# Optimization experiments

Measured on AMD Instinct MI355X. Metric: run time of the kernel, lower is better.

The kernel has to match this reference:

```python
import jax, jax.numpy as jnp
import numpy as np

C_ELEC = 322.0637  # Coulomb constant in Rosetta units


def _atom_maps(offsets, n_atoms):
    # offsets: [P,B] sorted block start indices -> (block id, within-block index) per atom
    a = jnp.arange(n_atoms)
    def one(off):
        blk = jnp.clip(jnp.searchsorted(off, a, side='right') - 1, 0, off.shape[0] - 1)
        return blk, a - off[blk]
    return jax.vmap(one)(offsets)


def _elec_pose_scores(coords, offsets, block_types, inter_bondsep,
                      bt_n_atoms, bt_partial_charge,
                      bt_inter_pd, bt_intra_pd, global_params):
    P, A, _ = coords.shape
    D, D0, S, min_dis, max_dis = (global_params[0, i] for i in range(5))
    blk, aw = _atom_maps(offsets, A)                      # [P,A]
    bt = jnp.take_along_axis(block_types, blk, axis=1)    # [P,A]
    q = bt_partial_charge[bt, aw]                         # [P,A]
    valid = aw < bt_n_atoms[bt]                           # [P,A]

    # representative-atom bonded path length between every atom pair
    d2c = bt_inter_pd[bt, :, aw]                          # [P,A,C] atom -> connection path dist
    bsep_i = inter_bondsep[jnp.arange(P)[:, None], blk]   # [P,A,B,C,C]
    tmp = jnp.min(d2c[:, :, None, :, None] + bsep_i, axis=3)     # [P,A,B,C] (min over conn_i)
    pidx = jnp.arange(P)[:, None, None]
    iidx = jnp.arange(A)[None, :, None]
    tmp_j = tmp[pidx, iidx, blk[:, None, :]]              # [P,A,A,C]
    bpl_inter = jnp.min(tmp_j + d2c[:, None, :, :], axis=-1)     # [P,A,A] (min over conn_j)
    bpl_intra = bt_intra_pd[bt[:, :, None], aw[:, :, None], aw[:, None, :]]  # [P,A,A]
    same_block = blk[:, :, None] == blk[:, None, :]
    bpl = jnp.where(same_block, bpl_intra, bpl_inter)
    # count-pair weight: >4 bonds -> 1.0, ==4 -> 0.2, <4 -> excluded
    cp = jnp.where(bpl > 4, 1.0, jnp.where(bpl == 4, 0.2, 0.0)).astype(coords.dtype)

    # pairwise distances via the x.x trick (avoids a [P,A,A,3] intermediate)
    sq = jnp.sum(coords * coords, axis=-1)
    d2 = sq[:, :, None] + sq[:, None, :] - 2.0 * jnp.einsum('pid,pjd->pij', coords, coords)
    dist = jnp.sqrt(jnp.maximum(d2, 1e-12))
    dc = jnp.clip(dist, min_dis, max_dis)

    def eps_sig(d):  # sigmoidal distance-dependent dielectric
        return D - 0.5 * (D - D0) * (2.0 + 2.0 * d * S + (d * S) ** 2) * jnp.exp(-d * S)

    shift = 1.0 / (max_dis * eps_sig(max_dis))  # so E(max_dis) == 0
    e = C_ELEC * q[:, :, None] * q[:, None, :] * (1.0 / (dc * eps_sig(dc)) - shift)
    e = jnp.where(dist >= max_dis, 0.0, e) * cp
    pair_mask = (jnp.triu(jnp.ones((A, A), dtype=bool), 1)[None]
                 & valid[:, :, None] & valid[:, None, :])
    return jnp.sum(jnp.where(pair_mask, e, 0.0), axis=(1, 2))  # [P] per-pose elec score


def setup_inputs() -> dict:
    key = jax.random.key(0)
    ks = jax.random.split(key, 6)
    P, B, APB, NBT, C = 4, 96, 16, 20, 2
    A = B * APB
    coords = jax.random.uniform(ks[0], (P, A, 3), jnp.float32) * 25.0  # ~protein density box
    offsets = jnp.tile((jnp.arange(B, dtype=jnp.int32) * APB)[None], (P, 1))
    block_types = jax.random.randint(ks[1], (P, B), 0, NBT, dtype=jnp.int32)
    bi = jnp.arange(B)
    adj = jnp.abs(bi[:, None] - bi[None, :])
    min_bsep = jnp.where(adj == 0, 0, jnp.where(adj == 1, 1, 6)).astype(jnp.int32)
    intra = jax.random.randint(ks[4], (NBT, APB, APB), 0, 7, dtype=jnp.int32)
    intra = jnp.minimum(intra, intra.transpose(0, 2, 1))
    intra = intra.at[:, jnp.arange(APB), jnp.arange(APB)].set(0)
    return {
        'coords': coords,
        'pose_stack_block_coord_offset': offsets,
        'pose_stack_block_types': block_types,
        'pose_stack_min_block_bondsep': jnp.tile(min_bsep[None], (P, 1, 1)),
        'pose_stack_inter_block_bondsep': jnp.tile(min_bsep[None, :, :, None, None], (P, 1, 1, C, C)),
        'bt_n_atoms': jnp.full((NBT,), APB, jnp.int32),
        'bt_partial_charge': jax.random.normal(ks[2], (NBT, APB), jnp.float32) * 0.4,
        'bt_n_interblock_bonds': jnp.full((NBT,), C, jnp.int32),
        'bt_atoms_forming_chemical_bonds': jnp.stack(
            [jnp.zeros(NBT, jnp.int32), jnp.full((NBT,), APB - 1, jnp.int32)], axis=1),
        'bt_inter_repr_path_distance': jax.random.randint(ks[3], (NBT, C, APB), 0, 7, dtype=jnp.int32),
        'bt_intra_repr_path_distance': intra,
        'global_params': jnp.array([[79.931, 6.648, 0.441546, 1.6, 5.5]], jnp.float32),
    }


def reference(coords, pose_stack_block_coord_offset, pose_stack_block_types,
              pose_stack_min_block_bondsep, pose_stack_inter_block_bondsep,
              bt_n_atoms, bt_partial_charge, bt_n_interblock_bonds,
              bt_atoms_forming_chemical_bonds, bt_inter_repr_path_distance,
              bt_intra_repr_path_distance, global_params):
    # min_block_bondsep / n_interblock_bonds / conn-atom indices are kernel-side
    # pruning hints; the dense reference computes identical energies without them.
    return _elec_pose_scores(coords, pose_stack_block_coord_offset,
                             pose_stack_block_types, pose_stack_inter_block_bondsep,
                             bt_n_atoms, bt_partial_charge,
                             bt_inter_repr_path_distance,
                             bt_intra_repr_path_distance, global_params)
```

## Files before the change

kernel.cpp:

```cpp
#include <hip/hip_runtime.h>
#include <math.h>

#define C_ELEC 322.0637f
#define TILE 64
#define CMAX 4
#define BMAX 256

__global__ void __launch_bounds__(256)
pair_kernel(const float* __restrict__ coords,
            const int* __restrict__ offsets,
            const int* __restrict__ block_types,
            const int* __restrict__ inter_bondsep,
            const int* __restrict__ bt_n_atoms,
            const float* __restrict__ bt_pc,
            const int* __restrict__ bt_ipd,
            const int* __restrict__ bt_xpd,
            const float* __restrict__ gp,
            float* __restrict__ partials,
            int P, int A, int B, int NBT, int APB, int C, int nt, int TP)
{
    __shared__ float4 s_posi[TILE], s_posj[TILE];
    __shared__ int4 s_meti[TILE], s_metj[TILE];
    __shared__ int4 s_bond[256];
    __shared__ int s_xpd[2048];
    __shared__ unsigned short s_list[TILE * TILE];
    __shared__ int s_off[BMAX];
    __shared__ int s_btype[BMAX];
    __shared__ int s_cnt;
    __shared__ float s_red[4];

    int bid = blockIdx.x;
    int p = bid / TP;
    int tp = bid - p * TP;
    int ti = 0, rem = tp;
    while (rem >= nt - ti) { rem -= nt - ti; ++ti; }
    int tj = ti + rem;
    int t = threadIdx.x;
    int ibase = ti * TILE, jbase = tj * TILE;
    bool diag = (ti == tj);
    bool bLds = (B <= BMAX);

    int nb = bLds ? B : BMAX;
    for (int i = t; i < nb; i += 256) {
        s_off[i] = offsets[(size_t)p * B + i];
        s_btype[i] = block_types[(size_t)p * B + i];
    }
    if (t == 0) s_cnt = 0;
    __syncthreads();

    if (t < 2 * TILE) {
        int local = t < TILE ? t : t - TILE;
        int a = (t < TILE) ? ibase + local : jbase + local;
        float4 pr; int4 mr;
        if (a >= A) {
            pr = make_float4(1e9f, 1e9f, 1e9f, 0.f);
            mr = make_int4(B - 1, 0, 0, 0);
        } else {
            const float* cp = coords + ((size_t)p * A + a) * 3;
            float x = cp[0], y = cp[1], z = cp[2];
            int lo = 0, hi = B;
            if (bLds) {
                while (lo < hi) { int mid = (lo + hi) >> 1; if (s_off[mid] <= a) lo = mid + 1; else hi = mid; }
            } else {
                const int* off = offsets + (size_t)p * B;
                while (lo < hi) { int mid = (lo + hi) >> 1; if (off[mid] <= a) lo = mid + 1; else hi = mid; }
            }
            int blk = lo - 1;
            blk = blk < 0 ? 0 : (blk > B - 1 ? B - 1 : blk);
            int aw = a - (bLds ? s_off[blk] : offsets[(size_t)p * B + blk]);
            int bt = bLds ? s_btype[blk] : block_types[(size_t)p * B + blk];
            bt = bt < 0 ? 0 : (bt >= NBT ? NBT - 1 : bt);
            int awc = aw < 0 ? 0 : (aw >= APB ? APB - 1 : aw);
            float q = bt_pc[(size_t)bt * APB + awc];
            int valid = (aw < bt_n_atoms[bt]) ? 1 : 0;
            int packed = 0;
            int Cc = C > CMAX ? CMAX : C;
            for (int c = 0; c < Cc; ++c)
                packed |= (bt_ipd[((size_t)bt * C + c) * APB + awc] & 0xff) << (8 * c);
            pr = make_float4(x, y, z, valid ? q : 0.f);
            mr = make_int4(blk, bt, awc, packed);
        }
        if (t < TILE) { s_posi[local] = pr; s_meti[local] = mr; }
        else          { s_posj[local] = pr; s_metj[local] = mr; }
    }
    __syncthreads();

    int bi0 = s_meti[0].x, bi1 = s_meti[TILE - 1].x;
    int bj0 = s_metj[0].x, bj1 = s_metj[TILE - 1].x;
    int ni = bi1 - bi0 + 1, nj = bj1 - bj0 + 1;
    int APB2 = APB * APB;

    bool bondC2 = (C == 2) && (ni * nj) <= 256;
    int ov0 = bi0 > bj0 ? bi0 : bj0;
    int ov1 = bi1 < bj1 ? bi1 : bj1;
    int nov = ov1 - ov0 + 1;
    bool xpdStaged = nov > 0 && (nov * APB2) <= 2048;

    if (bondC2) {
        int total = ni * nj;
        for (int idx = t; idx < total; idx += 256) {
            int bir = idx / nj, bjr = idx - bir * nj;
            s_bond[idx] = *(const int4*)(inter_bondsep +
                (((size_t)p * B + (bi0 + bir)) * B + (bj0 + bjr)) * 4);
        }
    }
    if (xpdStaged) {
        int total = nov * APB2;
        for (int idx = t; idx < total; idx += 256) {
            int b = idx / APB2, w = idx - b * APB2;
            int bt = bLds ? s_btype[ov0 + b] : block_types[(size_t)p * B + ov0 + b];
            bt = bt < 0 ? 0 : (bt >= NBT ? NBT - 1 : bt);
            s_xpd[idx] = bt_xpd[(size_t)bt * APB2 + w];
        }
    }
    __syncthreads();

    float D = gp[0], D0 = gp[1], S = gp[2], min_dis = gp[3], max_dis = gp[4];
    float max2 = max_dis * max_dis;
    float xm = max_dis * S;
    float esm = D - 0.5f * (D - D0) * (2.f + 2.f * xm + xm * xm) * __expf(-xm);
    float shift = 1.f / (max_dis * esm);
    int Cc = C > CMAX ? CMAX : C;

    int jj = t & (TILE - 1);
    int lo16 = (t >> 6) * 16;
    float4 pj = s_posj[jj];
    if (pj.w != 0.f) {
        for (int k = 0; k < 16; ++k) {
            int ii = lo16 + k;
            float4 pi = s_posi[ii];
            float dx = pi.x - pj.x, dy = pi.y - pj.y, dz = pi.z - pj.z;
            float d2 = dx * dx + dy * dy + dz * dz;
            bool ok = (d2 < max2) && (pi.w != 0.f);
            if (diag) ok = ok && (ii < jj);
            if (ok) {
                int slot = atomicAdd(&s_cnt, 1);
                s_list[slot] = (unsigned short)(ii | (jj << 6));
            }
        }
    }
    __syncthreads();
    int cnt = s_cnt;

    float acc = 0.f;
    for (int e = t; e < cnt; e += 256) {
        int ent = s_list[e];
        int ii = ent & 63, j2 = ent >> 6;
        float4 pi = s_posi[ii];
        float4 pjv = s_posj[j2];
        float dx = pi.x - pjv.x, dy = pi.y - pjv.y, dz = pi.z - pjv.z;
        float d2 = dx * dx + dy * dy + dz * dz;
        int4 mi = s_meti[ii];
        int4 mjv = s_metj[j2];
        int bi = mi.x, bj = mjv.x;
        int bpl;
        if (bi == bj) {
            bpl = xpdStaged ? s_xpd[(bi - ov0) * APB2 + mi.z * APB + mjv.z]
                            : bt_xpd[((size_t)mi.y * APB + mi.z) * APB + mjv.z];
        } else if (C == 2) {
            int4 b4 = bondC2 ? s_bond[(bi - bi0) * nj + (bj - bj0)]
                             : *(const int4*)(inter_bondsep +
                                   (((size_t)p * B + bi) * B + bj) * 4);
            int di0 = mi.w & 0xff, di1 = (mi.w >> 8) & 0xff;
            int dj0 = mjv.w & 0xff, dj1 = (mjv.w >> 8) & 0xff;
            bpl = min(min(di0 + b4.x + dj0, di0 + b4.y + dj1),
                      min(di1 + b4.z + dj0, di1 + b4.w + dj1));
        } else {
            const int* ib = inter_bondsep + (((size_t)p * B + bi) * B + bj) * C * C;
            int best = 0x7fffffff;
            for (int c1 = 0; c1 < Cc; ++c1) {
                int dic = (mi.w >> (8 * c1)) & 0xff;
                for (int c2 = 0; c2 < Cc; ++c2) {
                    int v = dic + ib[c1 * C + c2] + ((mjv.w >> (8 * c2)) & 0xff);
                    best = v < best ? v : best;
                }
            }
            bpl = best;
        }
        if (bpl < 4) continue;
        float cpv = bpl > 4 ? 1.f : 0.2f;
        float dist = sqrtf(fmaxf(d2, 1e-12f));
        float dc = fmaxf(dist, min_dis);
        float xs = dc * S;
        float es = D - 0.5f * (D - D0) * (2.f + 2.f * xs + xs * xs) * __expf(-xs);
        acc += C_ELEC * pi.w * pjv.w * (1.f / (dc * es) - shift) * cpv;
    }

    for (int off = 32; off; off >>= 1) acc += __shfl_down(acc, off, 64);
    if ((t & 63) == 0) s_red[t >> 6] = acc;
    __syncthreads();
    if (t == 0) partials[bid] = s_red[0] + s_red[1] + s_red[2] + s_red[3];
}

__global__ void __launch_bounds__(256)
reduce_kernel(const float* __restrict__ partials, float* __restrict__ out, int TP)
{
    int p = blockIdx.x;
    float acc = 0.f;
    for (int i = threadIdx.x; i < TP; i += 256) acc += partials[(size_t)p * TP + i];
    for (int off = 32; off; off >>= 1) acc += __shfl_down(acc, off, 64);
    __shared__ float s[4];
    if ((threadIdx.x & 63) == 0) s[threadIdx.x >> 6] = acc;
    __syncthreads();
    if (threadIdx.x == 0) out[p] = s[0] + s[1] + s[2] + s[3];
}

extern "C" void kernel_launch(void* const* d_in, const int* in_sizes, int n_in,
                              void* d_out, int out_size, void* d_ws, size_t ws_size,
                              hipStream_t stream) {
    const float* coords        = (const float*)d_in[0];
    const int*   offsets       = (const int*)d_in[1];
    const int*   block_types   = (const int*)d_in[2];
    const int*   inter_bondsep = (const int*)d_in[4];
    const int*   bt_n_atoms    = (const int*)d_in[5];
    const float* bt_pc         = (const float*)d_in[6];
    const int*   bt_ipd        = (const int*)d_in[9];
    const int*   bt_xpd        = (const int*)d_in[10];
    const float* gp            = (const float*)d_in[11];

    int NBT = in_sizes[5];
    int APB = in_sizes[6] / NBT;
    int PB  = in_sizes[1];
    int B   = in_sizes[3] / PB;
    int P   = PB / B;
    int A   = in_sizes[0] / (3 * P);
    int C2  = in_sizes[4] / in_sizes[3];
    int C   = 1;
    while (C * C < C2) ++C;

    int nt = (A + TILE - 1) / TILE;
    int TP = nt * (nt + 1) / 2;

    float* partials = (float*)d_ws;

    hipLaunchKernelGGL(pair_kernel, dim3(P * TP), dim3(256), 0, stream,
                       coords, offsets, block_types, inter_bondsep, bt_n_atoms,
                       bt_pc, bt_ipd, bt_xpd, gp, partials,
                       P, A, B, NBT, APB, C, nt, TP);
    hipLaunchKernelGGL(reduce_kernel, dim3(P), dim3(256), 0, stream,
                       partials, (float*)d_out, TP);
}
```

Before: 16.24 us.

## Process two tile pairs per block, reusing the i-tile and overlapping staging

Each workgroup now handles two consecutive upper-triangular tile pairs instead of one, halving the grid and the number of partial sums to reduce. When consecutive pairs share the same i-tile, the i-atom records are not reloaded. Block ranges are computed by binary search instead of read from shared memory, so bond and path-distance staging by the upper threads can run alongside atom record loading, which removes one barrier per tile. The cost is less parallelism across the GPU and serial work within each block.

```diff
diff --git a/kernel.cpp b/kernel.cpp
--- a/kernel.cpp
+++ b/kernel.cpp
@@ -5,6 +5,7 @@
 #define TILE 64
 #define CMAX 4
 #define BMAX 256
+#define JPB 2
 
 __global__ void __launch_bounds__(256)
 pair_kernel(const float* __restrict__ coords,
@@ -17,7 +18,7 @@
             const int* __restrict__ bt_xpd,
             const float* __restrict__ gp,
             float* __restrict__ partials,
-            int P, int A, int B, int NBT, int APB, int C, int nt, int TP)
+            int P, int A, int B, int NBT, int APB, int C, int nt, int TP, int TPH)
 {
     __shared__ float4 s_posi[TILE], s_posj[TILE];
     __shared__ int4 s_meti[TILE], s_metj[TILE];
@@ -29,175 +30,193 @@
     __shared__ int s_cnt;
     __shared__ float s_red[4];
 
-    int bid = blockIdx.x;
-    int p = bid / TP;
-    int tp = bid - p * TP;
-    int ti = 0, rem = tp;
-    while (rem >= nt - ti) { rem -= nt - ti; ++ti; }
-    int tj = ti + rem;
+    int bh = blockIdx.x;
+    int p = bh / TPH;
+    int hb = bh - p * TPH;
     int t = threadIdx.x;
-    int ibase = ti * TILE, jbase = tj * TILE;
-    bool diag = (ti == tj);
     bool bLds = (B <= BMAX);
+    int APB2 = APB * APB;
+    int Cc = C > CMAX ? CMAX : C;
 
     int nb = bLds ? B : BMAX;
     for (int i = t; i < nb; i += 256) {
         s_off[i] = offsets[(size_t)p * B + i];
         s_btype[i] = block_types[(size_t)p * B + i];
     }
-    if (t == 0) s_cnt = 0;
-    __syncthreads();
-
-    if (t < 2 * TILE) {
-        int local = t < TILE ? t : t - TILE;
-        int a = (t < TILE) ? ibase + local : jbase + local;
-        float4 pr; int4 mr;
-        if (a >= A) {
-            pr = make_float4(1e9f, 1e9f, 1e9f, 0.f);
-            mr = make_int4(B - 1, 0, 0, 0);
-        } else {
-            const float* cp = coords + ((size_t)p * A + a) * 3;
-            float x = cp[0], y = cp[1], z = cp[2];
-            int lo = 0, hi = B;
-            if (bLds) {
-                while (lo < hi) { int mid = (lo + hi) >> 1; if (s_off[mid] <= a) lo = mid + 1; else hi = mid; }
-            } else {
-                const int* off = offsets + (size_t)p * B;
-                while (lo < hi) { int mid = (lo + hi) >> 1; if (off[mid] <= a) lo = mid + 1; else hi = mid; }
-            }
-            int blk = lo - 1;
-            blk = blk < 0 ? 0 : (blk > B - 1 ? B - 1 : blk);
-            int aw = a - (bLds ? s_off[blk] : offsets[(size_t)p * B + blk]);
-            int bt = bLds ? s_btype[blk] : block_types[(size_t)p * B + blk];
-            bt = bt < 0 ? 0 : (bt >= NBT ? NBT - 1 : bt);
-            int awc = aw < 0 ? 0 : (aw >= APB ? APB - 1 : aw);
-            float q = bt_pc[(size_t)bt * APB + awc];
-            int valid = (aw < bt_n_atoms[bt]) ? 1 : 0;
-            int packed = 0;
-            int Cc = C > CMAX ? CMAX : C;
-            for (int c = 0; c < Cc; ++c)
-                packed |= (bt_ipd[((size_t)bt * C + c) * APB + awc] & 0xff) << (8 * c);
-            pr = make_float4(x, y, z, valid ? q : 0.f);
-            mr = make_int4(blk, bt, awc, packed);
-        }
-        if (t < TILE) { s_posi[local] = pr; s_meti[local] = mr; }
-        else          { s_posj[local] = pr; s_metj[local] = mr; }
-    }
-    __syncthreads();
-
-    int bi0 = s_meti[0].x, bi1 = s_meti[TILE - 1].x;
-    int bj0 = s_metj[0].x, bj1 = s_metj[TILE - 1].x;
-    int ni = bi1 - bi0 + 1, nj = bj1 - bj0 + 1;
-    int APB2 = APB * APB;
-
-    bool bondC2 = (C == 2) && (ni * nj) <= 256;
-    int ov0 = bi0 > bj0 ? bi0 : bj0;
-    int ov1 = bi1 < bj1 ? bi1 : bj1;
-    int nov = ov1 - ov0 + 1;
-    bool xpdStaged = nov > 0 && (nov * APB2) <= 2048;
-
-    if (bondC2) {
-        int total = ni * nj;
-        for (int idx = t; idx < total; idx += 256) {
-            int bir = idx / nj, bjr = idx - bir * nj;
-            s_bond[idx] = *(const int4*)(inter_bondsep +
-                (((size_t)p * B + (bi0 + bir)) * B + (bj0 + bjr)) * 4);
-        }
-    }
-    if (xpdStaged) {
-        int total = nov * APB2;
-        for (int idx = t; idx < total; idx += 256) {
-            int b = idx / APB2, w = idx - b * APB2;
-            int bt = bLds ? s_btype[ov0 + b] : block_types[(size_t)p * B + ov0 + b];
-            bt = bt < 0 ? 0 : (bt >= NBT ? NBT - 1 : bt);
-            s_xpd[idx] = bt_xpd[(size_t)bt * APB2 + w];
-        }
-    }
-    __syncthreads();
 
     float D = gp[0], D0 = gp[1], S = gp[2], min_dis = gp[3], max_dis = gp[4];
     float max2 = max_dis * max_dis;
     float xm = max_dis * S;
     float esm = D - 0.5f * (D - D0) * (2.f + 2.f * xm + xm * xm) * __expf(-xm);
     float shift = 1.f / (max_dis * esm);
-    int Cc = C > CMAX ? CMAX : C;
-
-    int jj = t & (TILE - 1);
-    int lo16 = (t >> 6) * 16;
-    float4 pj = s_posj[jj];
-    if (pj.w != 0.f) {
-        for (int k = 0; k < 16; ++k) {
-            int ii = lo16 + k;
+
+    auto blk_of = [&](int a) -> int {
+        if (a >= A) return B - 1;
+        int lo = 0, hi = B;
+        if (bLds) {
+            while (lo < hi) { int mid = (lo + hi) >> 1; if (s_off[mid] <= a) lo = mid + 1; else hi = mid; }
+        } else {
+            const int* off = offsets + (size_t)p * B;
+            while (lo < hi) { int mid = (lo + hi) >> 1; if (off[mid] <= a) lo = mid + 1; else hi = mid; }
+        }
+        int blk = lo - 1;
+        return blk < 0 ? 0 : (blk > B - 1 ? B - 1 : blk);
+    };
+
+    auto record = [&](int a, float4& pr, int4& mr) {
+        if (a >= A) {
+            pr = make_float4(1e9f, 1e9f, 1e9f, 0.f);
+            mr = make_int4(B - 1, 0, 0, 0);
+            return;
+        }
+        const float* cp = coords + ((size_t)p * A + a) * 3;
+        int blk = blk_of(a);
+        int aw = a - (bLds ? s_off[blk] : offsets[(size_t)p * B + blk]);
+        int bt = bLds ? s_btype[blk] : block_types[(size_t)p * B + blk];
+        bt = bt < 0 ? 0 : (bt >= NBT ? NBT - 1 : bt);
+        int awc = aw < 0 ? 0 : (aw >= APB ? APB - 1 : aw);
+        float q = bt_pc[(size_t)bt * APB + awc];
+        int valid = (aw < bt_n_atoms[bt]) ? 1 : 0;
+        int packed = 0;
+        for (int c = 0; c < Cc; ++c)
+            packed |= (bt_ipd[((size_t)bt * C + c) * APB + awc] & 0xff) << (8 * c);
+        pr = make_float4(cp[0], cp[1], cp[2], valid ? q : 0.f);
+        mr = make_int4(blk, bt, awc, packed);
+    };
+
+    float acc = 0.f;
+    int prev_ti = -1;
+
+    for (int g = 0; g < JPB; ++g) {
+        int tp = hb * JPB + g;
+        if (tp >= TP) break;
+        int ti = 0, rem = tp;
+        while (rem >= nt - ti) { rem -= nt - ti; ++ti; }
+        int tj = ti + rem;
+        int ibase = ti * TILE, jbase = tj * TILE;
+        bool diag = (ti == tj);
+        bool newI = (ti != prev_ti);
+        prev_ti = ti;
+
+        __syncthreads();
+
+        int bi0 = blk_of(ibase), bi1 = blk_of(ibase + TILE - 1);
+        int bj0 = blk_of(jbase), bj1 = blk_of(jbase + TILE - 1);
+        int ni = bi1 - bi0 + 1, nj = bj1 - bj0 + 1;
+        bool bondC2 = (C == 2) && (ni * nj) <= 256;
+        int ov0 = bi0 > bj0 ? bi0 : bj0;
+        int ov1 = bi1 < bj1 ? bi1 : bj1;
+        int nov = ov1 - ov0 + 1;
+        bool xpdStaged = nov > 0 && (nov * APB2) <= 2048;
+
+        if (t < TILE) {
+            if (newI) {
+                float4 pr; int4 mr;
+                record(ibase + t, pr, mr);
+                s_posi[t] = pr; s_meti[t] = mr;
+            }
+        } else if (t < 2 * TILE) {
+            float4 pr; int4 mr;
+            record(jbase + (t - TILE), pr, mr);
+            s_posj[t - TILE] = pr; s_metj[t - TILE] = mr;
+        } else {
+            if (t == 2 * TILE) s_cnt = 0;
+            if (bondC2) {
+                int total = ni * nj;
+                for (int idx = t - 128; idx < total; idx += 128) {
+                    int bir = idx / nj, bjr = idx - bir * nj;
+                    s_bond[idx] = *(const int4*)(inter_bondsep +
+                        (((size_t)p * B + (bi0 + bir)) * B + (bj0 + bjr)) * 4);
+                }
+            }
+            if (xpdStaged) {
+                int total = nov * APB2;
+                for (int idx = t - 128; idx < total; idx += 128) {
+                    int b = idx / APB2, w = idx - b * APB2;
+                    int bt = bLds ? s_btype[ov0 + b] : block_types[(size_t)p * B + ov0 + b];
+                    bt = bt < 0 ? 0 : (bt >= NBT ? NBT - 1 : bt);
+                    s_xpd[idx] = bt_xpd[(size_t)bt * APB2 + w];
+                }
+            }
+        }
+        __syncthreads();
+
+        int jj = t & (TILE - 1);
+        int lo16 = (t >> 6) * 16;
+        float4 pj = s_posj[jj];
+        if (pj.w != 0.f) {
+            for (int k = 0; k < 16; ++k) {
+                int ii = lo16 + k;
+                float4 pi = s_posi[ii];
+                float dx = pi.x - pj.x, dy = pi.y - pj.y, dz = pi.z - pj.z;
+                float d2 = dx * dx + dy * dy + dz * dz;
+                bool ok = (d2 < max2) && (pi.w != 0.f);
+                if (diag) ok = ok && (ii < jj);
+                if (ok) {
+                    int slot = atomicAdd(&s_cnt, 1);
+                    s_list[slot] = (unsigned short)(ii | (jj << 6));
+                }
+            }
+        }
+        __syncthreads();
+        int cnt = s_cnt;
+
+        for (int e = t; e < cnt; e += 256) {
+            int ent = s_list[e];
+            int ii = ent & 63, j2 = ent >> 6;
             float4 pi = s_posi[ii];
-            float dx = pi.x - pj.x, dy = pi.y - pj.y, dz = pi.z - pj.z;
+            float4 pjv = s_posj[j2];
+            float dx = pi.x - pjv.x, dy = pi.y - pjv.y, dz = pi.z - pjv.z;
             float d2 = dx * dx + dy * dy + dz * dz;
-            bool ok = (d2 < max2) && (pi.w != 0.f);
-            if (diag) ok = ok && (ii < jj);
-            if (ok) {
-                int slot = atomicAdd(&s_cnt, 1);
-                s_list[slot] = (unsigned short)(ii | (jj << 6));
-            }
-        }
-    }
-    __syncthreads();
-    int cnt = s_cnt;
-
-    float acc = 0.f;
-    for (int e = t; e < cnt; e += 256) {
-        int ent = s_list[e];
-        int ii = ent & 63, j2 = ent >> 6;
-        float4 pi = s_posi[ii];
-        float4 pjv = s_posj[j2];
-        float dx = pi.x - pjv.x, dy = pi.y - pjv.y, dz = pi.z - pjv.z;
-        float d2 = dx * dx + dy * dy + dz * dz;
-        int4 mi = s_meti[ii];
-        int4 mjv = s_metj[j2];
-        int bi = mi.x, bj = mjv.x;
-        int bpl;
-        if (bi == bj) {
-            bpl = xpdStaged ? s_xpd[(bi - ov0) * APB2 + mi.z * APB + mjv.z]
-                            : bt_xpd[((size_t)mi.y * APB + mi.z) * APB + mjv.z];
-        } else if (C == 2) {
-            int4 b4 = bondC2 ? s_bond[(bi - bi0) * nj + (bj - bj0)]
-                             : *(const int4*)(inter_bondsep +
-                                   (((size_t)p * B + bi) * B + bj) * 4);
-            int di0 = mi.w & 0xff, di1 = (mi.w >> 8) & 0xff;
-            int dj0 = mjv.w & 0xff, dj1 = (mjv.w >> 8) & 0xff;
-            bpl = min(min(di0 + b4.x + dj0, di0 + b4.y + dj1),
-                      min(di1 + b4.z + dj0, di1 + b4.w + dj1));
-        } else {
-            const int* ib = inter_bondsep + (((size_t)p * B + bi) * B + bj) * C * C;
-            int best = 0x7fffffff;
-            for (int c1 = 0; c1 < Cc; ++c1) {
-                int dic = (mi.w >> (8 * c1)) & 0xff;
-                for (int c2 = 0; c2 < Cc; ++c2) {
-                    int v = dic + ib[c1 * C + c2] + ((mjv.w >> (8 * c2)) & 0xff);
-                    best = v < best ? v : best;
-                }
-            }
-            bpl = best;
-        }
-        if (bpl < 4) continue;
-        float cpv = bpl > 4 ? 1.f : 0.2f;
-        float dist = sqrtf(fmaxf(d2, 1e-12f));
-        float dc = fmaxf(dist, min_dis);
-        float xs = dc * S;
-        float es = D - 0.5f * (D - D0) * (2.f + 2.f * xs + xs * xs) * __expf(-xs);
-        acc += C_ELEC * pi.w * pjv.w * (1.f / (dc * es) - shift) * cpv;
+            int4 mi = s_meti[ii];
+            int4 mjv = s_metj[j2];
+            int bi = mi.x, bj = mjv.x;
+            int bpl;
+            if (bi == bj) {
+                bpl = xpdStaged ? s_xpd[(bi - ov0) * APB2 + mi.z * APB + mjv.z]
+                                : bt_xpd[((size_t)mi.y * APB + mi.z) * APB + mjv.z];
+            } else if (C == 2) {
+                int4 b4 = bondC2 ? s_bond[(bi - bi0) * nj + (bj - bj0)]
+                                 : *(const int4*)(inter_bondsep +
+                                       (((size_t)p * B + bi) * B + bj) * 4);
+                int di0 = mi.w & 0xff, di1 = (mi.w >> 8) & 0xff;
+                int dj0 = mjv.w & 0xff, dj1 = (mjv.w >> 8) & 0xff;
+                bpl = min(min(di0 + b4.x + dj0, di0 + b4.y + dj1),
+                          min(di1 + b4.z + dj0, di1 + b4.w + dj1));
+            } else {
+                const int* ib = inter_bondsep + (((size_t)p * B + bi) * B + bj) * C * C;
+                int best = 0x7fffffff;
+                for (int c1 = 0; c1 < Cc; ++c1) {
+                    int dic = (mi.w >> (8 * c1)) & 0xff;
+                    for (int c2 = 0; c2 < Cc; ++c2) {
+                        int v = dic + ib[c1 * C + c2] + ((mjv.w >> (8 * c2)) & 0xff);
+                        best = v < best ? v : best;
+                    }
+                }
+                bpl = best;
+            }
+            if (bpl < 4) continue;
+            float cpv = bpl > 4 ? 1.f : 0.2f;
+            float dist = sqrtf(fmaxf(d2, 1e-12f));
+            float dc = fmaxf(dist, min_dis);
+            float xs = dc * S;
+            float es = D - 0.5f * (D - D0) * (2.f + 2.f * xs + xs * xs) * __expf(-xs);
+            acc += C_ELEC * pi.w * pjv.w * (1.f / (dc * es) - shift) * cpv;
+        }
     }
 
     for (int off = 32; off; off >>= 1) acc += __shfl_down(acc, off, 64);
     if ((t & 63) == 0) s_red[t >> 6] = acc;
     __syncthreads();
-    if (t == 0) partials[bid] = s_red[0] + s_red[1] + s_red[2] + s_red[3];
+    if (t == 0) partials[bh] = s_red[0] + s_red[1] + s_red[2] + s_red[3];
 }
 
 __global__ void __launch_bounds__(256)
-reduce_kernel(const float* __restrict__ partials, float* __restrict__ out, int TP)
+reduce_kernel(const float* __restrict__ partials, float* __restrict__ out, int TPH)
 {
     int p = blockIdx.x;
     float acc = 0.f;
-    for (int i = threadIdx.x; i < TP; i += 256) acc += partials[(size_t)p * TP + i];
+    for (int i = threadIdx.x; i < TPH; i += 256) acc += partials[(size_t)p * TPH + i];
     for (int off = 32; off; off >>= 1) acc += __shfl_down(acc, off, 64);
     __shared__ float s[4];
     if ((threadIdx.x & 63) == 0) s[threadIdx.x >> 6] = acc;
@@ -230,13 +249,14 @@
 
     int nt = (A + TILE - 1) / TILE;
     int TP = nt * (nt + 1) / 2;
+    int TPH = (TP + JPB - 1) / JPB;
 
     float* partials = (float*)d_ws;
 
-    hipLaunchKernelGGL(pair_kernel, dim3(P * TP), dim3(256), 0, stream,
+    hipLaunchKernelGGL(pair_kernel, dim3(P * TPH), dim3(256), 0, stream,
                        coords, offsets, block_types, inter_bondsep, bt_n_atoms,
                        bt_pc, bt_ipd, bt_xpd, gp, partials,
-                       P, A, B, NBT, APB, C, nt, TP);
+                       P, A, B, NBT, APB, C, nt, TP, TPH);
     hipLaunchKernelGGL(reduce_kernel, dim3(P), dim3(256), 0, stream,
-                       partials, (float*)d_out, TP);
+                       partials, (float*)d_out, TPH);
 }
```

After: 24.30 us. 1.5x slower.

## Scatter block ids per tile and overlap metadata staging with bond-table loads

Applied to the files above, without the earlier changes.

Threads now scan block ranges while loading offsets and write each tile atom's block id straight into shared arrays, which replaces the per-atom binary search. The block ranges for the tile are then available one barrier earlier. Warps 2-3 stage the inter-block bondsep and intra path-distance tables while warps 0-1 compute the per-atom metadata, which removes one __syncthreads and serialised phase. Coordinate and global-param loads are also issued earlier to hide their latency. The cost is that the staging work is now spread over 128 threads instead of 256, plus a small serial scatter loop per block.

```diff
diff --git a/kernel.cpp b/kernel.cpp
--- a/kernel.cpp
+++ b/kernel.cpp
@@ -26,6 +26,7 @@
     __shared__ unsigned short s_list[TILE * TILE];
     __shared__ int s_off[BMAX];
     __shared__ int s_btype[BMAX];
+    __shared__ unsigned short s_blki[TILE], s_blkj[TILE];
     __shared__ int s_cnt;
     __shared__ float s_red[4];
 
@@ -39,90 +40,110 @@
     int ibase = ti * TILE, jbase = tj * TILE;
     bool diag = (ti == tj);
     bool bLds = (B <= BMAX);
-
-    int nb = bLds ? B : BMAX;
-    for (int i = t; i < nb; i += 256) {
-        s_off[i] = offsets[(size_t)p * B + i];
-        s_btype[i] = block_types[(size_t)p * B + i];
-    }
+    size_t pB = (size_t)p * B;
+    int APB2 = APB * APB;
+    int Cc = C > CMAX ? CMAX : C;
+
+    int local = t & (TILE - 1);
+    int aMine = (t < TILE ? ibase : jbase) + local;
+    float cx = 1e9f, cyv = 1e9f, cz = 1e9f;
+    if (t < 2 * TILE && aMine < A) {
+        const float* cp = coords + ((size_t)p * A + aMine) * 3;
+        cx = cp[0]; cyv = cp[1]; cz = cp[2];
+    }
+    float D = gp[0], D0 = gp[1], S = gp[2], min_dis = gp[3], max_dis = gp[4];
+
     if (t == 0) s_cnt = 0;
-    __syncthreads();
+
+    if (bLds) {
+        for (int b = t; b < B; b += 256) {
+            int ob = offsets[pB + b];
+            int oe = (b == B - 1) ? 0x7fffffff : offsets[pB + b + 1];
+            s_off[b] = ob;
+            s_btype[b] = block_types[pB + b];
+            int st = (b == 0) ? 0 : ob;
+            int lo = st > ibase ? st : ibase;
+            int hi = oe < ibase + TILE ? oe : ibase + TILE;
+            for (int a = lo; a < hi; ++a) s_blki[a - ibase] = (unsigned short)b;
+            lo = st > jbase ? st : jbase;
+            hi = oe < jbase + TILE ? oe : jbase + TILE;
+            for (int a = lo; a < hi; ++a) s_blkj[a - jbase] = (unsigned short)b;
+        }
+    } else if (t < 2 * TILE) {
+        const int* off = offsets + pB;
+        int blk;
+        if (aMine >= A) blk = B - 1;
+        else {
+            int lo = 0, hi2 = B;
+            while (lo < hi2) { int mid = (lo + hi2) >> 1; if (off[mid] <= aMine) lo = mid + 1; else hi2 = mid; }
+            blk = lo - 1; blk = blk < 0 ? 0 : (blk > B - 1 ? B - 1 : blk);
+        }
+        if (t < TILE) s_blki[local] = (unsigned short)blk;
+        else          s_blkj[local] = (unsigned short)blk;
+    }
+    __syncthreads();
+
+    int ilastI = (A - 1 - ibase < TILE - 1) ? (A - 1 - ibase) : (TILE - 1);
+    int ilastJ = (A - 1 - jbase < TILE - 1) ? (A - 1 - jbase) : (TILE - 1);
+    int bi0 = s_blki[0], bi1 = (ilastI >= 0) ? s_blki[ilastI] : s_blki[0];
+    int bj0 = s_blkj[0], bj1 = (ilastJ >= 0) ? s_blkj[ilastJ] : s_blkj[0];
+    int ni = bi1 - bi0 + 1, nj = bj1 - bj0 + 1;
+    bool bondC2 = (C == 2) && ni > 0 && nj > 0 && (ni * nj) <= 256;
+    int ov0 = bi0 > bj0 ? bi0 : bj0;
+    int ov1 = bi1 < bj1 ? bi1 : bj1;
+    int nov = ov1 - ov0 + 1;
+    bool xpdStaged = nov > 0 && (nov * APB2) <= 2048;
 
     if (t < 2 * TILE) {
-        int local = t < TILE ? t : t - TILE;
-        int a = (t < TILE) ? ibase + local : jbase + local;
         float4 pr; int4 mr;
-        if (a >= A) {
+        if (aMine >= A) {
             pr = make_float4(1e9f, 1e9f, 1e9f, 0.f);
             mr = make_int4(B - 1, 0, 0, 0);
         } else {
-            const float* cp = coords + ((size_t)p * A + a) * 3;
-            float x = cp[0], y = cp[1], z = cp[2];
-            int lo = 0, hi = B;
-            if (bLds) {
-                while (lo < hi) { int mid = (lo + hi) >> 1; if (s_off[mid] <= a) lo = mid + 1; else hi = mid; }
-            } else {
-                const int* off = offsets + (size_t)p * B;
-                while (lo < hi) { int mid = (lo + hi) >> 1; if (off[mid] <= a) lo = mid + 1; else hi = mid; }
-            }
-            int blk = lo - 1;
-            blk = blk < 0 ? 0 : (blk > B - 1 ? B - 1 : blk);
-            int aw = a - (bLds ? s_off[blk] : offsets[(size_t)p * B + blk]);
-            int bt = bLds ? s_btype[blk] : block_types[(size_t)p * B + blk];
+            int blk = (t < TILE) ? (int)s_blki[local] : (int)s_blkj[local];
+            int ob = bLds ? s_off[blk] : offsets[pB + blk];
+            int bt = bLds ? s_btype[blk] : block_types[pB + blk];
             bt = bt < 0 ? 0 : (bt >= NBT ? NBT - 1 : bt);
+            int aw = aMine - ob;
             int awc = aw < 0 ? 0 : (aw >= APB ? APB - 1 : aw);
             float q = bt_pc[(size_t)bt * APB + awc];
             int valid = (aw < bt_n_atoms[bt]) ? 1 : 0;
             int packed = 0;
-            int Cc = C > CMAX ? CMAX : C;
             for (int c = 0; c < Cc; ++c)
                 packed |= (bt_ipd[((size_t)bt * C + c) * APB + awc] & 0xff) << (8 * c);
-            pr = make_float4(x, y, z, valid ? q : 0.f);
+            pr = make_float4(cx, cyv, cz, valid ? q : 0.f);
             mr = make_int4(blk, bt, awc, packed);
         }
         if (t < TILE) { s_posi[local] = pr; s_meti[local] = mr; }
         else          { s_posj[local] = pr; s_metj[local] = mr; }
-    }
-    __syncthreads();
-
-    int bi0 = s_meti[0].x, bi1 = s_meti[TILE - 1].x;
-    int bj0 = s_metj[0].x, bj1 = s_metj[TILE - 1].x;
-    int ni = bi1 - bi0 + 1, nj = bj1 - bj0 + 1;
-    int APB2 = APB * APB;
-
-    bool bondC2 = (C == 2) && (ni * nj) <= 256;
-    int ov0 = bi0 > bj0 ? bi0 : bj0;
-    int ov1 = bi1 < bj1 ? bi1 : bj1;
-    int nov = ov1 - ov0 + 1;
-    bool xpdStaged = nov > 0 && (nov * APB2) <= 2048;
-
-    if (bondC2) {
-        int total = ni * nj;
-        for (int idx = t; idx < total; idx += 256) {
-            int bir = idx / nj, bjr = idx - bir * nj;
-            s_bond[idx] = *(const int4*)(inter_bondsep +
-                (((size_t)p * B + (bi0 + bir)) * B + (bj0 + bjr)) * 4);
-        }
-    }
-    if (xpdStaged) {
-        int total = nov * APB2;
-        for (int idx = t; idx < total; idx += 256) {
-            int b = idx / APB2, w = idx - b * APB2;
-            int bt = bLds ? s_btype[ov0 + b] : block_types[(size_t)p * B + ov0 + b];
-            bt = bt < 0 ? 0 : (bt >= NBT ? NBT - 1 : bt);
-            s_xpd[idx] = bt_xpd[(size_t)bt * APB2 + w];
-        }
-    }
-    __syncthreads();
-
-    float D = gp[0], D0 = gp[1], S = gp[2], min_dis = gp[3], max_dis = gp[4];
+    } else {
+        int idx0 = t - 128;
+        if (bondC2) {
+            int total = ni * nj;
+            for (int idx = idx0; idx < total; idx += 128) {
+                int bir = idx / nj, bjr = idx - bir * nj;
+                s_bond[idx] = *(const int4*)(inter_bondsep +
+                    (((size_t)p * B + (bi0 + bir)) * B + (bj0 + bjr)) * 4);
+            }
+        }
+        if (xpdStaged) {
+            int total = nov * APB2;
+            for (int idx = idx0; idx < total; idx += 128) {
+                int b = idx / APB2, w = idx - b * APB2;
+                int bt = bLds ? s_btype[ov0 + b] : block_types[pB + ov0 + b];
+                bt = bt < 0 ? 0 : (bt >= NBT ? NBT - 1 : bt);
+                s_xpd[idx] = bt_xpd[(size_t)bt * APB2 + w];
+            }
+        }
+    }
+    __syncthreads();
+
     float max2 = max_dis * max_dis;
     float xm = max_dis * S;
     float esm = D - 0.5f * (D - D0) * (2.f + 2.f * xm + xm * xm) * __expf(-xm);
     float shift = 1.f / (max_dis * esm);
-    int Cc = C > CMAX ? CMAX : C;
-
-    int jj = t & (TILE - 1);
+
+    int jj = local;
     int lo16 = (t >> 6) * 16;
     float4 pj = s_posj[jj];
     if (pj.w != 0.f) {
```

New measurement: 16.73 us. 1.03x slower.
